# Optimization experiments

Hardware: AMD Instinct MI355X
Metric: run time of the kernel (lower is better)

Reference implementation:

```python
import jax, jax.numpy as jnp
import numpy as np
import math

B, I, H = 8192, 1024, 1024

def _uniform(key, shape, lo, hi):
    return jax.random.uniform(key, shape, dtype=jnp.float32, minval=lo, maxval=hi)

def setup_inputs() -> dict:
    key = jax.random.key(0)
    ks = jax.random.split(key, 14)
    bound = math.sqrt(1.0 / H)
    lo, hi = -bound, bound
    x = jax.random.normal(ks[0], (B, I), dtype=jnp.float32)
    hid = jax.random.normal(ks[1], (B, H), dtype=jnp.float32)
    # stacked params for gates [r, z, n]
    wx = jnp.stack([_uniform(ks[2 + i], (I, H), lo, hi) for i in range(3)])   # [3, I, H]
    wh = jnp.stack([_uniform(ks[5 + i], (H, H), lo, hi) for i in range(3)])   # [3, H, H]
    bx = jnp.stack([_uniform(ks[8 + i], (H,), lo, hi) for i in range(3)])     # [3, H]
    bh = jnp.stack([_uniform(ks[11 + i], (H,), lo, hi) for i in range(3)])    # [3, H]
    return {"x": x, "hid": hid, "wx": wx, "wh": wh, "bx": bx, "bh": bh}

def reference(x, hid, wx, wh, bx, bh):
    # Fused gate projections: one big matmul per source instead of 3 small ones.
    gx = jnp.einsum('bi,gih->bgh', x, wx) + bx[None]        # [B, 3, H]
    gh = jnp.einsum('bh,ghk->bgk', hid, wh) + bh[None]      # [B, 3, H]
    r = jax.nn.sigmoid(gx[:, 0] + gh[:, 0])
    z = jax.nn.sigmoid(gx[:, 1] + gh[:, 1])
    n = jnp.tanh(gx[:, 2] + r * gh[:, 2])
    next_hid = (1.0 - z) * n + z * hid
    return next_hid
```

## Files before the change

kernel.cpp:

```cpp
#include <hip/hip_runtime.h>
#include <hip/hip_bf16.h>

typedef __hip_bfloat16 bf16;
typedef unsigned short u16;
typedef __attribute__((ext_vector_type(8))) short bf16x8;
typedef __attribute__((ext_vector_type(4))) float f32x4;
typedef __attribute__((ext_vector_type(8))) unsigned short u16x8;

#define KD 1024
#define HD 1024
#define BSZ 8192
#define BM 128
#define BN 64
#define BK 32

#define WS_XB 12582912
#define WS_HB 29360128
#define WS_NEED 46137344ULL

__device__ __forceinline__ u16 f2b(float f) {
    return __builtin_bit_cast(u16, __float2bfloat16(f));
}

__device__ __forceinline__ void gload16(const void* g, u16* smem, int lds_byte_off) {
    __builtin_amdgcn_global_load_lds(
        (const __attribute__((address_space(1))) void*)g,
        (__attribute__((address_space(3))) void*)((char*)smem + lds_byte_off),
        16, 0, 0);
}

__global__ __launch_bounds__(256) void convert_xh(
    const float* __restrict__ x, const float* __restrict__ h,
    u16* __restrict__ xb, u16* __restrict__ hb)
{
    size_t off = ((size_t)blockIdx.x * 256 + threadIdx.x) * 8;
    float4 a0 = *(const float4*)(x + off);
    float4 a1 = *(const float4*)(x + off + 4);
    float4 b0 = *(const float4*)(h + off);
    float4 b1 = *(const float4*)(h + off + 4);
    u16x8 vx, vh;
    vx[0]=f2b(a0.x); vx[1]=f2b(a0.y); vx[2]=f2b(a0.z); vx[3]=f2b(a0.w);
    vx[4]=f2b(a1.x); vx[5]=f2b(a1.y); vx[6]=f2b(a1.z); vx[7]=f2b(a1.w);
    vh[0]=f2b(b0.x); vh[1]=f2b(b0.y); vh[2]=f2b(b0.z); vh[3]=f2b(b0.w);
    vh[4]=f2b(b1.x); vh[5]=f2b(b1.y); vh[6]=f2b(b1.z); vh[7]=f2b(b1.w);
    *(u16x8*)(xb + off) = vx;
    *(u16x8*)(hb + off) = vh;
}

__global__ __launch_bounds__(256) void transpose_w(
    const float* __restrict__ wx, const float* __restrict__ wh, u16* __restrict__ wt)
{
    __shared__ u16 tile[64][65];
    const int g = blockIdx.z;
    const float* src = (g < 3) ? (wx + (size_t)g * KD * HD) : (wh + (size_t)(g - 3) * KD * HD);
    u16* dst = wt + (size_t)g * KD * HD;
    const int r0 = blockIdx.y * 64;
    const int c0 = blockIdx.x * 64;
    const int t = threadIdx.x;

    #pragma unroll
    for (int r = 0; r < 2; r++) {
        int idx = r * 256 + t;
        int row = idx >> 3, cc = idx & 7;
        const float* p = src + (size_t)(r0 + row) * HD + c0 + cc * 8;
        #pragma unroll
        for (int e = 0; e < 8; e++) tile[row][cc * 8 + e] = f2b(p[e]);
    }
    __syncthreads();
    #pragma unroll
    for (int r = 0; r < 2; r++) {
        int idx = r * 256 + t;
        int nrow = idx >> 3, kc = idx & 7;
        u16x8 v;
        #pragma unroll
        for (int e = 0; e < 8; e++) v[e] = tile[kc * 8 + e][nrow];
        *(u16x8*)(dst + (size_t)(c0 + nrow) * KD + r0 + kc * 8) = v;
    }
}

__device__ __forceinline__ void gru_epilogue(
    f32x4 (&acc)[4][4][2], const float* __restrict__ bxf, const float* __restrict__ bhf,
    const float* __restrict__ hidf, float* __restrict__ outf,
    int m0, int n0, int wm, int wn, int quad, int c16)
{
    float bR[2], bZ[2], bXN[2], bHN[2];
    #pragma unroll
    for (int j = 0; j < 2; j++) {
        int col = n0 + wn * 32 + j * 16 + c16;
        bR[j]  = bxf[col]          + bhf[col];
        bZ[j]  = bxf[HD + col]     + bhf[HD + col];
        bXN[j] = bxf[2 * HD + col];
        bHN[j] = bhf[2 * HD + col];
    }
    #pragma unroll
    for (int i = 0; i < 4; i++)
        #pragma unroll
        for (int j = 0; j < 2; j++) {
            int col = n0 + wn * 32 + j * 16 + c16;
            #pragma unroll
            for (int r = 0; r < 4; r++) {
                int row = m0 + wm * 64 + i * 16 + quad * 4 + r;
                size_t idx = (size_t)row * HD + col;
                float vr = acc[0][i][j][r] + bR[j];
                vr = 1.f / (1.f + __expf(-vr));
                float vz = acc[1][i][j][r] + bZ[j];
                vz = 1.f / (1.f + __expf(-vz));
                float vn = (acc[2][i][j][r] + bXN[j]) + vr * (acc[3][i][j][r] + bHN[j]);
                float e2 = __expf(2.f * vn);
                vn = 1.f - 2.f / (e2 + 1.f);
                float o = (1.f - vz) * vn + vz * hidf[idx];
                outf[idx] = o;
            }
        }
}

__global__ __launch_bounds__(256, 2) void gru_fused_fast(
    const u16* __restrict__ xb, const u16* __restrict__ hb,
    const u16* __restrict__ wt,
    const float* __restrict__ bxf, const float* __restrict__ bhf,
    const float* __restrict__ hidf, float* __restrict__ outf)
{
    __shared__ u16 smem[20480];
    const int t    = threadIdx.x;
    const int lane = t & 63;
    const int w    = t >> 6;
    const int wm   = w >> 1, wn = w & 1;
    const int quad = lane >> 4;
    const int c16  = lane & 15;
    const int lin  = blockIdx.x;
    const int nblk = (lin & 7) * 2 + ((lin >> 3) & 1);
    const int mblk = lin >> 4;
    const int m0   = mblk * BM;
    const int n0   = nblk * BN;

    const int row4 = t >> 2;
    const int e8   = (t & 3) * 8;
    const u16* gx0 = xb + (size_t)(m0 + row4) * KD + e8;
    const u16* gx1 = gx0 + (size_t)64 * KD;
    const u16* gh0 = hb + (size_t)(m0 + row4) * KD + e8;
    const u16* gh1 = gh0 + (size_t)64 * KD;
    const u16* gw0 = wt + (size_t)(n0 + row4) * KD + e8;
    const int ldsl = w * 1024;

    f32x4 acc[4][4][2];
    #pragma unroll
    for (int a = 0; a < 4; a++)
        #pragma unroll
        for (int i = 0; i < 4; i++)
            #pragma unroll
            for (int j = 0; j < 2; j++)
                acc[a][i][j] = (f32x4){0.f, 0.f, 0.f, 0.f};

    for (int k0 = 0; k0 < KD; k0 += BK) {
        gload16(gx0, smem, ldsl);
        gload16(gx1, smem, 4096 + ldsl);
        gload16(gh0, smem, 8192 + ldsl);
        gload16(gh1, smem, 12288 + ldsl);
        #pragma unroll
        for (int g = 0; g < 6; g++)
            gload16(gw0 + (size_t)g * KD * HD, smem, 16384 + g * 4096 + ldsl);
        __syncthreads();
        gx0 += BK; gx1 += BK; gh0 += BK; gh1 += BK; gw0 += BK;

        bf16x8 ax[4], ah[4];
        #pragma unroll
        for (int i = 0; i < 4; i++) {
            int ml = wm * 64 + i * 16 + c16;
            ax[i] = *(const bf16x8*)&smem[ml * BK + quad * 8];
            ah[i] = *(const bf16x8*)&smem[4096 + ml * BK + quad * 8];
        }
        #pragma unroll
        for (int p = 0; p < 3; p++) {
            bf16x8 bwx[2], bwh[2];
            #pragma unroll
            for (int j = 0; j < 2; j++) {
                int nl = wn * 32 + j * 16 + c16;
                bwx[j] = *(const bf16x8*)&smem[8192 + p * 2048       + nl * BK + quad * 8];
                bwh[j] = *(const bf16x8*)&smem[8192 + (p + 3) * 2048 + nl * BK + quad * 8];
            }
            #pragma unroll
            for (int i = 0; i < 4; i++)
                #pragma unroll
                for (int j = 0; j < 2; j++) {
                    if (p < 2) {
                        acc[p][i][j] = __builtin_amdgcn_mfma_f32_16x16x32_bf16(ax[i], bwx[j], acc[p][i][j], 0, 0, 0);
                        acc[p][i][j] = __builtin_amdgcn_mfma_f32_16x16x32_bf16(ah[i], bwh[j], acc[p][i][j], 0, 0, 0);
                    } else {
                        acc[2][i][j] = __builtin_amdgcn_mfma_f32_16x16x32_bf16(ax[i], bwx[j], acc[2][i][j], 0, 0, 0);
                        acc[3][i][j] = __builtin_amdgcn_mfma_f32_16x16x32_bf16(ah[i], bwh[j], acc[3][i][j], 0, 0, 0);
                    }
                }
        }
        __syncthreads();
    }

    gru_epilogue(acc, bxf, bhf, hidf, outf, m0, n0, wm, wn, quad, c16);
}

__global__ __launch_bounds__(256, 2) void gru_fused_slow(
    const float* __restrict__ xf, const float* __restrict__ hf,
    const u16* __restrict__ wt,
    const float* __restrict__ bxf, const float* __restrict__ bhf,
    float* __restrict__ outf)
{
    __shared__ u16 smem[20480];
    const int t    = threadIdx.x;
    const int lane = t & 63;
    const int w    = t >> 6;
    const int wm   = w >> 1, wn = w & 1;
    const int quad = lane >> 4;
    const int c16  = lane & 15;
    const int lin  = blockIdx.x;
    const int nblk = (lin & 7) * 2 + ((lin >> 3) & 1);
    const int mblk = lin >> 4;
    const int m0   = mblk * BM;
    const int n0   = nblk * BN;
    const int row4 = t >> 2;
    const int e8   = (t & 3) * 8;
    const u16* gw0 = wt + (size_t)(n0 + row4) * KD + e8;
    const int ldsl = w * 1024;

    f32x4 acc[4][4][2];
    #pragma unroll
    for (int a = 0; a < 4; a++)
        #pragma unroll
        for (int i = 0; i < 4; i++)
            #pragma unroll
            for (int j = 0; j < 2; j++)
                acc[a][i][j] = (f32x4){0.f, 0.f, 0.f, 0.f};

    for (int k0 = 0; k0 < KD; k0 += BK) {
        #pragma unroll
        for (int g = 0; g < 6; g++)
            gload16(gw0 + (size_t)g * KD * HD, smem, 16384 + g * 4096 + ldsl);
        gw0 += BK;
        #pragma unroll
        for (int s = 0; s < 2; s++) {
            size_t gidx = (size_t)(m0 + s * 64 + row4) * KD + k0 + e8;
            const float* px = xf + gidx;
            const float* ph = hf + gidx;
            u16x8 vx, vh;
            #pragma unroll
            for (int e = 0; e < 8; e++) { vx[e] = f2b(px[e]); vh[e] = f2b(ph[e]); }
            *(u16x8*)&smem[s * 2048 + t * 8] = vx;
            *(u16x8*)&smem[4096 + s * 2048 + t * 8] = vh;
        }
        __syncthreads();

        bf16x8 ax[4], ah[4];
        #pragma unroll
        for (int i = 0; i < 4; i++) {
            int ml = wm * 64 + i * 16 + c16;
            ax[i] = *(const bf16x8*)&smem[ml * BK + quad * 8];
            ah[i] = *(const bf16x8*)&smem[4096 + ml * BK + quad * 8];
        }
        #pragma unroll
        for (int p = 0; p < 3; p++) {
            bf16x8 bwx[2], bwh[2];
            #pragma unroll
            for (int j = 0; j < 2; j++) {
                int nl = wn * 32 + j * 16 + c16;
                bwx[j] = *(const bf16x8*)&smem[8192 + p * 2048       + nl * BK + quad * 8];
                bwh[j] = *(const bf16x8*)&smem[8192 + (p + 3) * 2048 + nl * BK + quad * 8];
            }
            #pragma unroll
            for (int i = 0; i < 4; i++)
                #pragma unroll
                for (int j = 0; j < 2; j++) {
                    if (p < 2) {
                        acc[p][i][j] = __builtin_amdgcn_mfma_f32_16x16x32_bf16(ax[i], bwx[j], acc[p][i][j], 0, 0, 0);
                        acc[p][i][j] = __builtin_amdgcn_mfma_f32_16x16x32_bf16(ah[i], bwh[j], acc[p][i][j], 0, 0, 0);
                    } else {
                        acc[2][i][j] = __builtin_amdgcn_mfma_f32_16x16x32_bf16(ax[i], bwx[j], acc[2][i][j], 0, 0, 0);
                        acc[3][i][j] = __builtin_amdgcn_mfma_f32_16x16x32_bf16(ah[i], bwh[j], acc[3][i][j], 0, 0, 0);
                    }
                }
        }
        __syncthreads();
    }

    gru_epilogue(acc, bxf, bhf, hf, outf, m0, n0, wm, wn, quad, c16);
}

extern "C" void kernel_launch(void* const* d_in, const int* in_sizes, int n_in,
                              void* d_out, int out_size, void* d_ws, size_t ws_size,
                              hipStream_t stream) {
    const float* x   = (const float*)d_in[0];
    const float* hid = (const float*)d_in[1];
    const float* wx  = (const float*)d_in[2];
    const float* wh  = (const float*)d_in[3];
    const float* bx  = (const float*)d_in[4];
    const float* bh  = (const float*)d_in[5];
    float* out = (float*)d_out;

    char* ws = (char*)d_ws;
    u16* wt = (u16*)ws;
    u16* xb = (u16*)(ws + WS_XB);
    u16* hb = (u16*)(ws + WS_HB);

    dim3 tgrid(HD / 64, KD / 64, 6);
    transpose_w<<<tgrid, 256, 0, stream>>>(wx, wh, wt);

    if (ws_size >= WS_NEED) {
        convert_xh<<<4096, 256, 0, stream>>>(x, hid, xb, hb);
        gru_fused_fast<<<1024, 256, 0, stream>>>(xb, hb, wt, bx, bh, hid, out);
    } else {
        gru_fused_slow<<<1024, 256, 0, stream>>>(x, hid, wt, bx, bh, out);
    }
}
```

Baseline: 249.0 us.

## Double-buffer LDS tiles in fast GRU kernel to overlap loads with MFMA

Doubles the shared-memory buffer in the fast fused GRU kernel and restructures the K loop into a prologue plus a software pipeline. The next K-step's global-to-LDS loads are issued while the current step's MFMAs run. This removes one barrier per iteration and hides load latency. The cost is twice the LDS per block, which may reduce occupancy. The compute body is factored into a helper that the slow path also uses.

```diff
diff --git a/kernel.cpp b/kernel.cpp
--- a/kernel.cpp
+++ b/kernel.cpp
@@ -114,13 +114,60 @@
         }
 }
 
+__device__ __forceinline__ void kstep_stage(
+    const u16* gx0, const u16* gx1, const u16* gh0, const u16* gh1,
+    const u16* gw0, u16* smem, int bufb, int ldsl)
+{
+    gload16(gx0, smem, bufb + ldsl);
+    gload16(gx1, smem, bufb + 4096 + ldsl);
+    gload16(gh0, smem, bufb + 8192 + ldsl);
+    gload16(gh1, smem, bufb + 12288 + ldsl);
+    #pragma unroll
+    for (int g = 0; g < 6; g++)
+        gload16(gw0 + (size_t)g * KD * HD, smem, bufb + 16384 + g * 4096 + ldsl);
+}
+
+__device__ __forceinline__ void kstep_compute(
+    const u16* sm, f32x4 (&acc)[4][4][2], int wm, int wn, int quad, int c16)
+{
+    bf16x8 ax[4], ah[4];
+    #pragma unroll
+    for (int i = 0; i < 4; i++) {
+        int ml = wm * 64 + i * 16 + c16;
+        ax[i] = *(const bf16x8*)&sm[ml * BK + quad * 8];
+        ah[i] = *(const bf16x8*)&sm[4096 + ml * BK + quad * 8];
+    }
+    #pragma unroll
+    for (int p = 0; p < 3; p++) {
+        bf16x8 bwx[2], bwh[2];
+        #pragma unroll
+        for (int j = 0; j < 2; j++) {
+            int nl = wn * 32 + j * 16 + c16;
+            bwx[j] = *(const bf16x8*)&sm[8192 + p * 2048       + nl * BK + quad * 8];
+            bwh[j] = *(const bf16x8*)&sm[8192 + (p + 3) * 2048 + nl * BK + quad * 8];
+        }
+        #pragma unroll
+        for (int i = 0; i < 4; i++)
+            #pragma unroll
+            for (int j = 0; j < 2; j++) {
+                if (p < 2) {
+                    acc[p][i][j] = __builtin_amdgcn_mfma_f32_16x16x32_bf16(ax[i], bwx[j], acc[p][i][j], 0, 0, 0);
+                    acc[p][i][j] = __builtin_amdgcn_mfma_f32_16x16x32_bf16(ah[i], bwh[j], acc[p][i][j], 0, 0, 0);
+                } else {
+                    acc[2][i][j] = __builtin_amdgcn_mfma_f32_16x16x32_bf16(ax[i], bwx[j], acc[2][i][j], 0, 0, 0);
+                    acc[3][i][j] = __builtin_amdgcn_mfma_f32_16x16x32_bf16(ah[i], bwh[j], acc[3][i][j], 0, 0, 0);
+                }
+            }
+    }
+}
+
 __global__ __launch_bounds__(256, 2) void gru_fused_fast(
     const u16* __restrict__ xb, const u16* __restrict__ hb,
     const u16* __restrict__ wt,
     const float* __restrict__ bxf, const float* __restrict__ bhf,
     const float* __restrict__ hidf, float* __restrict__ outf)
 {
-    __shared__ u16 smem[20480];
+    __shared__ u16 smem[40960];
     const int t    = threadIdx.x;
     const int lane = t & 63;
     const int w    = t >> 6;
@@ -151,48 +198,19 @@
             for (int j = 0; j < 2; j++)
                 acc[a][i][j] = (f32x4){0.f, 0.f, 0.f, 0.f};
 
-    for (int k0 = 0; k0 < KD; k0 += BK) {
-        gload16(gx0, smem, ldsl);
-        gload16(gx1, smem, 4096 + ldsl);
-        gload16(gh0, smem, 8192 + ldsl);
-        gload16(gh1, smem, 12288 + ldsl);
-        #pragma unroll
-        for (int g = 0; g < 6; g++)
-            gload16(gw0 + (size_t)g * KD * HD, smem, 16384 + g * 4096 + ldsl);
+    const int NT = KD / BK;
+
+    kstep_stage(gx0, gx1, gh0, gh1, gw0, smem, 0, ldsl);
+    gx0 += BK; gx1 += BK; gh0 += BK; gh1 += BK; gw0 += BK;
+    __syncthreads();
+
+    for (int tt = 0; tt < NT - 1; ++tt) {
+        kstep_stage(gx0, gx1, gh0, gh1, gw0, smem, ((tt + 1) & 1) * 40960, ldsl);
+        gx0 += BK; gx1 += BK; gh0 += BK; gh1 += BK; gw0 += BK;
+        kstep_compute(smem + (tt & 1) * 20480, acc, wm, wn, quad, c16);
         __syncthreads();
-        gx0 += BK; gx1 += BK; gh0 += BK; gh1 += BK; gw0 += BK;
-
-        bf16x8 ax[4], ah[4];
-        #pragma unroll
-        for (int i = 0; i < 4; i++) {
-            int ml = wm * 64 + i * 16 + c16;
-            ax[i] = *(const bf16x8*)&smem[ml * BK + quad * 8];
-            ah[i] = *(const bf16x8*)&smem[4096 + ml * BK + quad * 8];
-        }
-        #pragma unroll
-        for (int p = 0; p < 3; p++) {
-            bf16x8 bwx[2], bwh[2];
-            #pragma unroll
-            for (int j = 0; j < 2; j++) {
-                int nl = wn * 32 + j * 16 + c16;
-                bwx[j] = *(const bf16x8*)&smem[8192 + p * 2048       + nl * BK + quad * 8];
-                bwh[j] = *(const bf16x8*)&smem[8192 + (p + 3) * 2048 + nl * BK + quad * 8];
-            }
-            #pragma unroll
-            for (int i = 0; i < 4; i++)
-                #pragma unroll
-                for (int j = 0; j < 2; j++) {
-                    if (p < 2) {
-                        acc[p][i][j] = __builtin_amdgcn_mfma_f32_16x16x32_bf16(ax[i], bwx[j], acc[p][i][j], 0, 0, 0);
-                        acc[p][i][j] = __builtin_amdgcn_mfma_f32_16x16x32_bf16(ah[i], bwh[j], acc[p][i][j], 0, 0, 0);
-                    } else {
-                        acc[2][i][j] = __builtin_amdgcn_mfma_f32_16x16x32_bf16(ax[i], bwx[j], acc[2][i][j], 0, 0, 0);
-                        acc[3][i][j] = __builtin_amdgcn_mfma_f32_16x16x32_bf16(ah[i], bwh[j], acc[3][i][j], 0, 0, 0);
-                    }
-                }
-        }
-        __syncthreads();
-    }
+    }
+    kstep_compute(smem + 20480, acc, wm, wn, quad, c16);
 
     gru_epilogue(acc, bxf, bhf, hidf, outf, m0, n0, wm, wn, quad, c16);
 }
@@ -246,36 +264,7 @@
             *(u16x8*)&smem[4096 + s * 2048 + t * 8] = vh;
         }
         __syncthreads();
-
-        bf16x8 ax[4], ah[4];
-        #pragma unroll
-        for (int i = 0; i < 4; i++) {
-            int ml = wm * 64 + i * 16 + c16;
-            ax[i] = *(const bf16x8*)&smem[ml * BK + quad * 8];
-            ah[i] = *(const bf16x8*)&smem[4096 + ml * BK + quad * 8];
-        }
-        #pragma unroll
-        for (int p = 0; p < 3; p++) {
-            bf16x8 bwx[2], bwh[2];
-            #pragma unroll
-            for (int j = 0; j < 2; j++) {
-                int nl = wn * 32 + j * 16 + c16;
-                bwx[j] = *(const bf16x8*)&smem[8192 + p * 2048       + nl * BK + quad * 8];
-                bwh[j] = *(const bf16x8*)&smem[8192 + (p + 3) * 2048 + nl * BK + quad * 8];
-            }
-            #pragma unroll
-            for (int i = 0; i < 4; i++)
-                #pragma unroll
-                for (int j = 0; j < 2; j++) {
-                    if (p < 2) {
-                        acc[p][i][j] = __builtin_amdgcn_mfma_f32_16x16x32_bf16(ax[i], bwx[j], acc[p][i][j], 0, 0, 0);
-                        acc[p][i][j] = __builtin_amdgcn_mfma_f32_16x16x32_bf16(ah[i], bwh[j], acc[p][i][j], 0, 0, 0);
-                    } else {
-                        acc[2][i][j] = __builtin_amdgcn_mfma_f32_16x16x32_bf16(ax[i], bwx[j], acc[2][i][j], 0, 0, 0);
-                        acc[3][i][j] = __builtin_amdgcn_mfma_f32_16x16x32_bf16(ah[i], bwh[j], acc[3][i][j], 0, 0, 0);
-                    }
-                }
-        }
+        kstep_compute(smem, acc, wm, wn, quad, c16);
         __syncthreads();
     }
 
```

New measurement: 243.6 us. -2.2%, faster.
